# Kernel tuning notes

Measured on AMD Instinct MI355X. Metric: run time of the kernel, lower is better.

## Reference

```python
import math
import jax, jax.numpy as jnp
import numpy as np

NUM_HEADS = 8
EMBED_DIM = 512   # embed_dim_per_head(64) * num_heads(8)
LATENT = 256
HIDDEN = 512
INPUT_DIM = 128
P = 3             # function 'Q' -> 3 polynomial coefficients


def setup_inputs() -> dict:
    key = jax.random.key(0)
    ks = jax.random.split(key, 16)
    B, L, T, D, E = 64, 2048, 1024, INPUT_DIM, EMBED_DIM
    s = lambda fan_in: 1.0 / math.sqrt(fan_in)
    inp = {
        "timesteps": jax.random.uniform(ks[0], (B, L), jnp.float32),
        "X": jax.random.normal(ks[1], (B, L, D), jnp.float32),
        "M": jax.random.bernoulli(ks[2], 0.5, (B, L, D)).astype(jnp.float32),
        "y_time_steps": jax.random.uniform(ks[3], (B, T), jnp.float32),
        # time_embedding: Linear(1, E)
        "w_te": jax.random.normal(ks[4], (E,), jnp.float32),
        "b_te": jnp.zeros((E,), jnp.float32),
        # learned query [1, P, E]
        "query": jax.random.normal(ks[5], (1, P, E), jnp.float32),
        # query_map / key_map: Linear(E, E), stored [in, out]
        "W_q": jax.random.normal(ks[6], (E, E), jnp.float32) * s(E),
        "b_q": jnp.zeros((E,), jnp.float32),
        "W_k": jax.random.normal(ks[7], (E, E), jnp.float32) * s(E),
        "b_k": jnp.zeros((E,), jnp.float32),
        # attn out: Linear(2*D*H, latent)
        "W_o": jax.random.normal(ks[8], (2 * D * NUM_HEADS, LATENT), jnp.float32) * s(2 * D * NUM_HEADS),
        "b_o": jnp.zeros((LATENT,), jnp.float32),
        # decoder MLP: latent -> hidden -> hidden -> D
        "W1": jax.random.normal(ks[9], (LATENT, HIDDEN), jnp.float32) * s(LATENT),
        "b1": jnp.zeros((HIDDEN,), jnp.float32),
        "W2": jax.random.normal(ks[10], (HIDDEN, HIDDEN), jnp.float32) * s(HIDDEN),
        "b2": jnp.zeros((HIDDEN,), jnp.float32),
        "W3": jax.random.normal(ks[11], (HIDDEN, D), jnp.float32) * s(HIDDEN),
        "b3": jnp.zeros((D,), jnp.float32),
    }
    return inp


def _fld_forward(timesteps, X, M, y_time_steps, w_te, b_te, query,
                 W_q, b_q, W_k, b_k, W_o, b_o, W1, b1, W2, b2, W3, b3):
    B, L = timesteps.shape
    D = X.shape[-1]
    E, H = EMBED_DIM, NUM_HEADS
    ek = E // H
    # learn_time_embedding: Linear(1,E) then sin on indices range(0, E, H)
    key = timesteps[..., None] * w_te + b_te                      # [B,L,E]
    sin_mask = (jnp.arange(E) % H) == 0
    key = jnp.where(sin_mask, jnp.sin(key), key)
    Xcat = jnp.concatenate([X, M], axis=-1)                       # [B,L,2D]
    Mcat = jnp.concatenate([M, M], axis=-1)                       # [B,L,2D]
    # mask is used only for masked_fill in torch (no grad through it)
    maskb = jax.lax.stop_gradient((Mcat != 0).astype(Xcat.dtype))
    q = jnp.broadcast_to(query, (B, P, E)) @ W_q + b_q            # [B,P,E]
    k = key @ W_k + b_k                                            # [B,L,E]
    qh = q.reshape(B, P, H, ek).transpose(0, 2, 1, 3)             # [B,H,P,ek]
    kh = k.reshape(B, L, H, ek).transpose(0, 2, 1, 3)             # [B,H,L,ek]
    scores = jnp.einsum('bhpe,bhle->bhpl', qh, kh) / math.sqrt(ek)
    # per-channel masked softmax over L, factorized (masked entries -> exp(-1e9)=0)
    m = jnp.max(scores, axis=-1, keepdims=True)
    w = jnp.exp(scores - m)                                        # [B,H,P,L]
    num = jnp.einsum('bhpl,blc->bhpc', w, maskb * Xcat)            # [B,H,P,2D]
    den = jnp.einsum('bhpl,blc->bhpc', w, maskb)
    x = num / den                                                  # [B,H,P,2D]
    x = x.transpose(0, 2, 1, 3).reshape(B, P, H * 2 * D)
    coeffs = x @ W_o + b_o                                         # [B,P,latent]
    t = y_time_steps[..., None]                                    # [B,T,1]
    c0 = coeffs[:, 0:1, :]
    c1 = coeffs[:, 1:2, :]
    c2 = coeffs[:, 2:3, :]
    z = c0 + t * c1 + (t * t) * c2                                 # [B,T,latent]
    h1 = jax.nn.relu(z @ W1 + b1)
    h2 = jax.nn.relu(h1 @ W2 + b2)
    return h2 @ W3 + b3                                            # [B,T,D]


def reference(timesteps, X, M, y_time_steps, w_te, b_te, query,
              W_q, b_q, W_k, b_k, W_o, b_o, W1, b1, W2, b2, W3, b3):
    return _fld_forward(timesteps, X, M, y_time_steps, w_te, b_te, query,
                        W_q, b_q, W_k, b_k, W_o, b_o, W1, b1, W2, b2, W3, b3)
```

## Files before the change

### kernel.cpp

```cpp
#include <hip/hip_runtime.h>
#include <math.h>

#define NH   8
#define PP   3
#define HP   24
#define E    512
#define EK   64
#define D    128
#define LL   2048
#define BB   64
#define TT   1024
#define LAT  256
#define HID  512
#define CH   8
#define CL   256

typedef __attribute__((ext_vector_type(8))) short bf16x8;
typedef __attribute__((ext_vector_type(4))) float f32x4;
typedef __attribute__((ext_vector_type(16))) float f32x16;

#define OFF_VS     ((size_t)2048)
#define OFF_WA     ((size_t)4096)
#define OFF_WB     ((size_t)4128)
#define OFF_SB     ((size_t)4160)
#define OFF_CVP    ((size_t)73728)
#define OFF_P2     ((size_t)81920)
#define OFF_PART   ((size_t)475136)
#define OFF_SC     ((size_t)3620864)
#define OFF_A      ((size_t)3784704)

__device__ inline ushort f2bf(float x) {
    union { float f; uint u; } v; v.f = x;
    uint r = v.u + 0x7fffu + ((v.u >> 16) & 1u);
    return (ushort)(r >> 16);
}
__device__ inline uint swz(uint a)  { return a ^ (((a >> 8) & 7u) << 4); }
__device__ inline uint swzH(uint a) { return a ^ (((a >> 7) & 7u) << 4); }
__device__ inline uint swzQ(uint a) { return a ^ (((a >> 9) & 7u) << 4); }
__device__ inline uint pk2(float lo, float hi) {
    return (uint)f2bf(lo) | ((uint)f2bf(hi) << 16);
}
__device__ inline float h1f(float a0, float a1, float a2, float t) {
    return fmaxf(fmaf(t, fmaf(t, a2, a1), a0), 0.f);
}
__device__ inline int sigma(int s) { return s ^ (((((s >> 2) ^ (s >> 3)) & 1)) ? 12 : 0); }

__global__ __launch_bounds__(512) void k_setup(const float* __restrict__ query,
                                               const float* __restrict__ W_q,
                                               const float* __restrict__ b_q,
                                               const float* __restrict__ W_k,
                                               const float* __restrict__ b_k,
                                               const float* __restrict__ w_te,
                                               const float* __restrict__ b_te,
                                               const float* __restrict__ W_o,
                                               const float* __restrict__ W2,
                                               const float* __restrict__ W3,
                                               float* __restrict__ vsin,
                                               float* __restrict__ wA,
                                               float* __restrict__ wB,
                                               float* __restrict__ sbias,
                                               float* __restrict__ cvp,
                                               ushort* __restrict__ W2F,
                                               ushort* __restrict__ W3F) {
    int bx = blockIdx.x, tid = threadIdx.x;
    if (bx < HP) {
        int hp = bx, h = hp / PP, p = hp % PP;
        __shared__ float q_s[EK];
        if (tid < EK) {
            float acc = b_q[h * EK + tid];
            for (int i = 0; i < E; ++i)
                acc += query[p * E + i] * W_q[(size_t)i * E + h * EK + tid];
            q_s[tid] = acc;
        }
        __syncthreads();
        int e = tid;
        const float scale = 0.125f;
        float acc = 0.f;
        for (int j = 0; j < EK; ++j)
            acc += W_k[(size_t)e * E + h * EK + j] * q_s[j];
        float v = acc * scale;
        if ((e & 7) == 0) vsin[hp * 64 + (e >> 3)] = v;
        __shared__ float r1[512], r2[512];
        r1[e] = v * w_te[e];
        r2[e] = v * b_te[e];
        __syncthreads();
        for (int s = 256; s > 0; s >>= 1) {
            if (e < s) { r1[e] += r1[e + s]; r2[e] += r2[e + s]; }
            __syncthreads();
        }
        if (e == 0) {
            wA[hp] = r1[0];
            wB[hp] = r2[0];
            float sb = 0.f;
            for (int j = 0; j < EK; ++j) sb += b_k[h * EK + j] * q_s[j];
            sbias[hp] = sb * scale;
        }
    } else if (bx < HP + 32) {
        int bc = bx - HP;
        int h = bc >> 2, cc = bc & 3, o = tid & 255;
        float acc = 0.f;
        #pragma unroll 8
        for (int c = cc * 32; c < cc * 32 + 32; ++c)
            acc += W_o[(size_t)(h * 256 + 128 + c) * LAT + o];
        cvp[(h * 4 + cc) * LAT + o] = acc;
    } else {
        int gid = (bx - HP - 32) * 512 + tid;
        int l = gid & 63;
        int kb = 8 * (l >> 5);
        int cb = l & 31;
        if (gid < 32768) {
            int F = gid >> 6;
            int JT = F & 15, ks = F >> 4;
            int cbp = sigma(cb);
            int k0 = ks * 16 + kb, j = JT * 32 + cbp;
            #pragma unroll
            for (int e = 0; e < 8; ++e)
                W2F[(size_t)gid * 8 + e] = f2bf(W2[(size_t)(k0 + e) * HID + j]);
        } else {
            int g2 = gid - 32768;
            int F2 = g2 >> 6;
            int CT = F2 & 3, KT = F2 >> 2;
            int k0 = KT * 16 + kb, c = CT * 32 + cb;
            #pragma unroll
            for (int e = 0; e < 8; ++e)
                W3F[(size_t)g2 * 8 + e] = f2bf(W3[(size_t)(k0 + e) * D + c]);
        }
    }
}

__global__ __launch_bounds__(512, 6) void k_wsf(const float* __restrict__ timesteps,
                                                const float* __restrict__ w_te,
                                                const float* __restrict__ b_te,
                                                const float* __restrict__ vsin,
                                                const float* __restrict__ wA,
                                                const float* __restrict__ wB,
                                                const float* __restrict__ sb,
                                                const float* __restrict__ X,
                                                const float* __restrict__ M,
                                                float* __restrict__ part) {
    __shared__ char sbuf[49152];
    float* vs_s = (float*)sbuf;
    float* w8_s = (float*)(sbuf + 6144);
    float* b8_s = (float*)(sbuf + 6400);
    float* wA_s = (float*)(sbuf + 6656);
    float* wB_s = (float*)(sbuf + 6784);
    float* sb_s = (float*)(sbuf + 6912);
    ushort* vt  = (ushort*)sbuf;
    ushort* w_s = (ushort*)(sbuf + 32768);
    int b = blockIdx.x / CH, ch = blockIdx.x % CH;
    int l0 = ch * CL;
    int tid = threadIdx.x;

    for (int i = tid; i < HP * 64; i += 512) vs_s[i] = vsin[i];
    if (tid < 64) { w8_s[tid] = w_te[tid * 8]; b8_s[tid] = b_te[tid * 8]; }
    if (tid < HP) { wA_s[tid] = wA[tid]; wB_s[tid] = wB[tid]; sb_s[tid] = sb[tid]; }
    __syncthreads();

    {
        int lpair = tid & 127, hh = tid >> 7;
        float ts0 = timesteps[(size_t)b * LL + l0 + lpair * 2];
        float ts1 = timesteps[(size_t)b * LL + l0 + lpair * 2 + 1];
        float sc0[6], sc1[6];
        #pragma unroll
        for (int i = 0; i < 6; ++i) {
            int hp = hh * 6 + i;
            sc0[i] = fmaf(ts0, wA_s[hp], wB_s[hp]) + sb_s[hp];
            sc1[i] = fmaf(ts1, wA_s[hp], wB_s[hp]) + sb_s[hp];
        }
        for (int jc = 0; jc < 64; jc += 8) {
            float d0[8], d1[8];
            #pragma unroll
            for (int j = 0; j < 8; ++j) {
                float w = w8_s[jc + j], bb = b8_s[jc + j];
                float k0 = fmaf(ts0, w, bb), k1 = fmaf(ts1, w, bb);
                d0[j] = __sinf(k0) - k0;
                d1[j] = __sinf(k1) - k1;
            }
            #pragma unroll
            for (int i = 0; i < 6; ++i) {
                int hp = hh * 6 + i;
                #pragma unroll
                for (int j = 0; j < 8; j += 4) {
                    float4 v4 = *(const float4*)&vs_s[hp * 64 + jc + j];
                    sc0[i] += d0[j] * v4.x + d0[j+1] * v4.y + d0[j+2] * v4.z + d0[j+3] * v4.w;
                    sc1[i] += d1[j] * v4.x + d1[j+1] * v4.y + d1[j+2] * v4.z + d1[j+3] * v4.w;
                }
            }
        }
        #pragma unroll
        for (int i = 0; i < 6; ++i) {
            int hp = hh * 6 + i;
            *(uint*)((char*)w_s + swzQ((uint)(hp * 512 + lpair * 4))) = pk2(__expf(sc0[i]), __expf(sc1[i]));
        }
        for (int idx = tid; idx < 8 * 128; idx += 512) {
            int hp = 24 + (idx >> 7), lp = idx & 127;
            *(uint*)((char*)w_s + swzQ((uint)(hp * 512 + lp * 4))) = 0u;
        }
    }
    __syncthreads();

    int lane = tid & 63, wv = tid >> 6;
    int l31 = lane & 31, hl = lane >> 5;
    f32x16 acc;
    #pragma unroll
    for (int e = 0; e < 16; ++e) acc[e] = 0.f;

    int cst = tid & 127, lg = tid >> 7;
    for (int q = 0; q < 4; ++q) {
        if (q) __syncthreads();
        #pragma unroll
        for (int i = 0; i < 8; ++i) {
            int ll = lg * 16 + i * 2;
            size_t g0 = ((size_t)b * LL + l0 + q * 64 + ll) * D + cst;
            float m0 = M[g0], m1 = M[g0 + D];
            float x0 = X[g0] * m0, x1 = X[g0 + D] * m1;
            *(uint*)((char*)vt + swzH((uint)(cst * 128 + ll * 2)))         = pk2(x0, x1);
            *(uint*)((char*)vt + swzH((uint)((128 + cst) * 128 + ll * 2))) = pk2(m0, m1);
        }
        __syncthreads();
        #pragma unroll
        for (int ks = 0; ks < 4; ++ks) {
            bf16x8 af = *(const bf16x8*)((char*)w_s + swzQ((uint)(l31 * 512 + (q * 64 + ks * 16 + hl * 8) * 2)));
            bf16x8 bf_ = *(const bf16x8*)((char*)vt + swzH((uint)((wv * 32 + l31) * 128 + (ks * 16 + hl * 8) * 2)));
            acc = __builtin_amdgcn_mfma_f32_32x32x16_bf16(af, bf_, acc, 0, 0, 0);
        }
    }
    size_t base = ((size_t)(b * CH + ch) * HP) * 256;
    #pragma unroll
    for (int reg = 0; reg < 12; ++reg) {
        int hp = (reg & 3) + 8 * (reg >> 2) + 4 * hl;
        part[base + (size_t)hp * 256 + wv * 32 + l31] = acc[reg];
    }
}

__global__ __launch_bounds__(256) void k_mid(const float* __restrict__ part,
                                             const float* __restrict__ W_o,
                                             float* __restrict__ part2) {
    int bx = blockIdx.x, tid = threadIdx.x;
    int b = bx >> 3, h = bx & 7;
    __shared__ float ratio[PP][D];
    for (int ii = tid; ii < PP * D; ii += 256) {
        int p = ii >> 7, c = ii & 127;
        int hp = h * PP + p;
        float n = 0.f, d = 0.f;
        for (int ch = 0; ch < CH; ++ch) {
            size_t base = ((size_t)(b * CH + ch) * HP + hp) * 256;
            n += part[base + c];
            d += part[base + 128 + c];
        }
        ratio[p][c] = n / d;
    }
    __syncthreads();
    int o = tid;
    float a0 = 0.f, a1 = 0.f, a2 = 0.f;
    #pragma unroll 4
    for (int c = 0; c < D; ++c) {
        float w = W_o[(size_t)(h * 256 + c) * LAT + o];
        a0 = fmaf(ratio[0][c], w, a0);
        a1 = fmaf(ratio[1][c], w, a1);
        a2 = fmaf(ratio[2][c], w, a2);
    }
    size_t base = (((size_t)b * NH + h) * PP) * LAT + o;
    part2[base]           = a0;
    part2[base + LAT]     = a1;
    part2[base + 2 * LAT] = a2;
}

__global__ __launch_bounds__(128) void k_avec4(const float* __restrict__ part2,
                                               const float* __restrict__ cvp,
                                               const float* __restrict__ b_o,
                                               const float* __restrict__ W1,
                                               const float* __restrict__ b1,
                                               float* __restrict__ abuf) {
    int b = blockIdx.x, jq = blockIdx.y, tid = threadIdx.x;
    __shared__ float cf[PP * LAT];
    for (int idx = tid; idx < PP * LAT; idx += 128) {
        int p = idx / LAT, o = idx % LAT;
        float s = b_o[o];
        #pragma unroll 8
        for (int i = 0; i < 32; ++i) s += cvp[i * LAT + o];
        for (int h = 0; h < NH; ++h)
            s += part2[(((size_t)b * NH + h) * PP + p) * LAT + o];
        cf[p * LAT + o] = s;
    }
    __syncthreads();
    int j = jq * 128 + tid;
    float a0 = b1[j], a1 = 0.f, a2 = 0.f;
    #pragma unroll 4
    for (int k = 0; k < LAT; ++k) {
        float w = W1[(size_t)k * HID + j];
        a0 = fmaf(cf[k], w, a0);
        a1 = fmaf(cf[LAT + k], w, a1);
        a2 = fmaf(cf[2 * LAT + k], w, a2);
    }
    abuf[(size_t)b * 3 * HID + j] = a0;
    abuf[(size_t)b * 3 * HID + HID + j] = a1;
    abuf[(size_t)b * 3 * HID + 2 * HID + j] = a2;
}

__global__ __launch_bounds__(512, 4) void k_mlp12(const float* __restrict__ abuf,
                                                  const float* __restrict__ yts,
                                                  const ushort* __restrict__ W2F,
                                                  const float* __restrict__ b2,
                                                  const ushort* __restrict__ W3F,
                                                  const float* __restrict__ b3,
                                                  float* __restrict__ out) {
    __shared__ char lds[65536];
    int b = blockIdx.x, t0 = blockIdx.y * 64, tid = threadIdx.x;
    const float* a0p = abuf + (size_t)b * 3 * HID;
    const float* a1p = a0p + HID;
    const float* a2p = a1p + HID;

    {
        int sr = tid & 63, sub0 = (tid >> 6) & 1, skp = tid >> 7;
        float t = yts[(size_t)b * TT + t0 + sr];
        int kg0 = skp * 128 + sub0 * 64;
        uint sbase = (uint)(skp * 16384 + sr * 256 + sub0 * 128);
        #pragma unroll
        for (int i = 0; i < 8; ++i) {
            int k = kg0 + i * 8;
            float4 xa0 = *(const float4*)(a0p + k), xb0 = *(const float4*)(a0p + k + 4);
            float4 xa1 = *(const float4*)(a1p + k), xb1 = *(const float4*)(a1p + k + 4);
            float4 xa2 = *(const float4*)(a2p + k), xb2 = *(const float4*)(a2p + k + 4);
            uint4 pk;
            pk.x = pk2(h1f(xa0.x, xa1.x, xa2.x, t), h1f(xa0.y, xa1.y, xa2.y, t));
            pk.y = pk2(h1f(xa0.z, xa1.z, xa2.z, t), h1f(xa0.w, xa1.w, xa2.w, t));
            pk.z = pk2(h1f(xb0.x, xb1.x, xb2.x, t), h1f(xb0.y, xb1.y, xb2.y, t));
            pk.w = pk2(h1f(xb0.z, xb1.z, xb2.z, t), h1f(xb0.w, xb1.w, xb2.w, t));
            *(uint4*)(lds + swz(sbase + i * 16)) = pk;
        }
    }
    __syncthreads();

    int lane = tid & 63, w = tid >> 6;
    int l31 = lane & 31, hl = lane >> 5;
    int wp = w & 1, gw = w >> 1;
    int Jb = gw * 4 + wp * 2;

    f32x16 acc[2][2];
    #pragma unroll
    for (int jt = 0; jt < 2; ++jt) {
        int jT = (Jb + jt) * 32;
        #pragma unroll
        for (int reg = 0; reg < 16; ++reg) {
            int slot = (reg & 3) + 8 * (reg >> 2) + 4 * hl;
            float bv = b2[jT + sigma(slot)];
            acc[jt][0][reg] = bv;
            acc[jt][1][reg] = bv;
        }
    }
    #pragma unroll 4
    for (int ks = 0; ks < 32; ++ks) {
        uint base = (uint)((ks >> 3) * 16384 + (ks & 7) * 32 + hl * 16);
        bf16x8 bh0 = *(const bf16x8*)(lds + swz(base + (uint)(l31 * 256)));
        bf16x8 bh1 = *(const bf16x8*)(lds + swz(base + (uint)((32 + l31) * 256)));
        #pragma unroll
        for (int jt = 0; jt < 2; ++jt) {
            bf16x8 af = *(const bf16x8*)(W2F + ((size_t)(ks * 16 + Jb + jt) * 64 + lane) * 8);
            acc[jt][0] = __builtin_amdgcn_mfma_f32_32x32x16_bf16(af, bh0, acc[jt][0], 0, 0, 0);
            acc[jt][1] = __builtin_amdgcn_mfma_f32_32x32x16_bf16(af, bh1, acc[jt][1], 0, 0, 0);
        }
    }
    __syncthreads();

    #pragma unroll
    for (int jt = 0; jt < 2; ++jt) {
        int J = Jb + jt;
        #pragma unroll
        for (int rtile = 0; rtile < 2; ++rtile)
            #pragma unroll
            for (int s = 0; s < 2; ++s) {
                uint4 uu;
                uu.x = pk2(fmaxf(acc[jt][rtile][8 * s + 0], 0.f), fmaxf(acc[jt][rtile][8 * s + 1], 0.f));
                uu.y = pk2(fmaxf(acc[jt][rtile][8 * s + 2], 0.f), fmaxf(acc[jt][rtile][8 * s + 3], 0.f));
                uu.z = pk2(fmaxf(acc[jt][rtile][8 * s + 4], 0.f), fmaxf(acc[jt][rtile][8 * s + 5], 0.f));
                uu.w = pk2(fmaxf(acc[jt][rtile][8 * s + 6], 0.f), fmaxf(acc[jt][rtile][8 * s + 7], 0.f));
                *(uint4*)(lds + (uint)((rtile * 32 + J * 2 + s) * 1024 + lane * 16)) = uu;
            }
    }
    __syncthreads();

    f32x16 acc2a, acc2b;
    {
        float bv = b3[gw * 32 + l31];
        #pragma unroll
        for (int e = 0; e < 16; ++e) { acc2a[e] = bv; acc2b[e] = 0.f; }
    }
    #pragma unroll 4
    for (int sg = 0; sg < 32; sg += 2) {
        {
            bf16x8 ah = *(const bf16x8*)(lds + (uint)((wp * 32 + sg) * 1024 + lane * 16));
            bf16x8 bw = *(const bf16x8*)(W3F + ((size_t)(sg * 4 + gw) * 64 + lane) * 8);
            acc2a = __builtin_amdgcn_mfma_f32_32x32x16_bf16(ah, bw, acc2a, 0, 0, 0);
        }
        {
            bf16x8 ah = *(const bf16x8*)(lds + (uint)((wp * 32 + sg + 1) * 1024 + lane * 16));
            bf16x8 bw = *(const bf16x8*)(W3F + ((size_t)((sg + 1) * 4 + gw) * 64 + lane) * 8);
            acc2b = __builtin_amdgcn_mfma_f32_32x32x16_bf16(ah, bw, acc2b, 0, 0, 0);
        }
    }

    {
        int c = gw * 32 + l31;
        size_t rowbase = (size_t)b * TT + t0 + wp * 32 + 4 * hl;
        #pragma unroll
        for (int reg = 0; reg < 16; ++reg)
            out[(rowbase + (reg & 3) + 8 * (reg >> 2)) * D + c] = acc2a[reg] + acc2b[reg];
    }
}

extern "C" void kernel_launch(void* const* d_in, const int* in_sizes, int n_in,
                              void* d_out, int out_size, void* d_ws, size_t ws_size,
                              hipStream_t stream) {
    const float* timesteps = (const float*)d_in[0];
    const float* X        = (const float*)d_in[1];
    const float* M        = (const float*)d_in[2];
    const float* yts      = (const float*)d_in[3];
    const float* w_te     = (const float*)d_in[4];
    const float* b_te     = (const float*)d_in[5];
    const float* query    = (const float*)d_in[6];
    const float* W_q      = (const float*)d_in[7];
    const float* b_q      = (const float*)d_in[8];
    const float* W_k      = (const float*)d_in[9];
    const float* b_k      = (const float*)d_in[10];
    const float* W_o      = (const float*)d_in[11];
    const float* b_o      = (const float*)d_in[12];
    const float* W1       = (const float*)d_in[13];
    const float* b1       = (const float*)d_in[14];
    const float* W2       = (const float*)d_in[15];
    const float* b2       = (const float*)d_in[16];
    const float* W3       = (const float*)d_in[17];
    const float* b3       = (const float*)d_in[18];
    float* out = (float*)d_out;
    float* ws  = (float*)d_ws;

    float* vsin   = ws + OFF_VS;
    float* wA     = ws + OFF_WA;
    float* wB     = ws + OFF_WB;
    float* sbias  = ws + OFF_SB;
    float* cvp    = ws + OFF_CVP;
    float* part2  = ws + OFF_P2;
    float* part   = ws + OFF_PART;
    float* abuf   = ws + OFF_A;
    ushort* W2F   = (ushort*)(ws + OFF_SC);
    ushort* W3F   = W2F + (size_t)HID * HID;

    hipLaunchKernelGGL(k_setup,  dim3(HP + 32 + 80),  dim3(512), 0, stream,
                       query, W_q, b_q, W_k, b_k, w_te, b_te, W_o, W2, W3,
                       vsin, wA, wB, sbias, cvp, W2F, W3F);
    hipLaunchKernelGGL(k_wsf,    dim3(BB * CH),       dim3(512), 0, stream,
                       timesteps, w_te, b_te, vsin, wA, wB, sbias, X, M, part);
    hipLaunchKernelGGL(k_mid,    dim3(BB * NH),       dim3(256), 0, stream,
                       part, W_o, part2);
    hipLaunchKernelGGL(k_avec4,  dim3(BB, 4),         dim3(128), 0, stream,
                       part2, cvp, b_o, W1, b1, abuf);
    hipLaunchKernelGGL(k_mlp12,  dim3(BB, TT / 64),   dim3(512), 0, stream,
                       abuf, yts, W2F, b2, W3F, b3, out);
}
```

Before: 159.7 us.

## Split sequence into 16 chunks per batch and store partial sums in bf16

```diff
diff --git a/kernel.cpp b/kernel.cpp
--- a/kernel.cpp
+++ b/kernel.cpp
@@ -12,11 +12,9 @@
 #define TT   1024
 #define LAT  256
 #define HID  512
-#define CH   8
-#define CL   256
+#define CH2  16
 
 typedef __attribute__((ext_vector_type(8))) short bf16x8;
-typedef __attribute__((ext_vector_type(4))) float f32x4;
 typedef __attribute__((ext_vector_type(16))) float f32x16;
 
 #define OFF_VS     ((size_t)2048)
@@ -34,9 +32,12 @@
     uint r = v.u + 0x7fffu + ((v.u >> 16) & 1u);
     return (ushort)(r >> 16);
 }
+__device__ inline float bf2f(ushort u) {
+    union { uint u; float f; } v; v.u = (uint)u << 16;
+    return v.f;
+}
 __device__ inline uint swz(uint a)  { return a ^ (((a >> 8) & 7u) << 4); }
 __device__ inline uint swzH(uint a) { return a ^ (((a >> 7) & 7u) << 4); }
-__device__ inline uint swzQ(uint a) { return a ^ (((a >> 9) & 7u) << 4); }
 __device__ inline uint pk2(float lo, float hi) {
     return (uint)f2bf(lo) | ((uint)f2bf(hi) << 16);
 }
@@ -128,17 +129,17 @@
     }
 }
 
-__global__ __launch_bounds__(512, 6) void k_wsf(const float* __restrict__ timesteps,
-                                                const float* __restrict__ w_te,
-                                                const float* __restrict__ b_te,
-                                                const float* __restrict__ vsin,
-                                                const float* __restrict__ wA,
-                                                const float* __restrict__ wB,
-                                                const float* __restrict__ sb,
-                                                const float* __restrict__ X,
-                                                const float* __restrict__ M,
-                                                float* __restrict__ part) {
-    __shared__ char sbuf[49152];
+__global__ __launch_bounds__(512, 8) void k_wsf2(const float* __restrict__ timesteps,
+                                                 const float* __restrict__ w_te,
+                                                 const float* __restrict__ b_te,
+                                                 const float* __restrict__ vsin,
+                                                 const float* __restrict__ wA,
+                                                 const float* __restrict__ wB,
+                                                 const float* __restrict__ sb,
+                                                 const float* __restrict__ X,
+                                                 const float* __restrict__ M,
+                                                 ushort* __restrict__ part) {
+    __shared__ char sbuf[40960];
     float* vs_s = (float*)sbuf;
     float* w8_s = (float*)(sbuf + 6144);
     float* b8_s = (float*)(sbuf + 6400);
@@ -147,8 +148,8 @@
     float* sb_s = (float*)(sbuf + 6912);
     ushort* vt  = (ushort*)sbuf;
     ushort* w_s = (ushort*)(sbuf + 32768);
-    int b = blockIdx.x / CH, ch = blockIdx.x % CH;
-    int l0 = ch * CL;
+    int b = blockIdx.x >> 4, ch = blockIdx.x & 15;
+    int l0 = ch * 128;
     int tid = threadIdx.x;
 
     for (int i = tid; i < HP * 64; i += 512) vs_s[i] = vsin[i];
@@ -157,13 +158,13 @@
     __syncthreads();
 
     {
-        int lpair = tid & 127, hh = tid >> 7;
+        int lpair = tid & 63, hh = tid >> 6;
         float ts0 = timesteps[(size_t)b * LL + l0 + lpair * 2];
         float ts1 = timesteps[(size_t)b * LL + l0 + lpair * 2 + 1];
-        float sc0[6], sc1[6];
-        #pragma unroll
-        for (int i = 0; i < 6; ++i) {
-            int hp = hh * 6 + i;
+        float sc0[3], sc1[3];
+        #pragma unroll
+        for (int i = 0; i < 3; ++i) {
+            int hp = hh * 3 + i;
             sc0[i] = fmaf(ts0, wA_s[hp], wB_s[hp]) + sb_s[hp];
             sc1[i] = fmaf(ts1, wA_s[hp], wB_s[hp]) + sb_s[hp];
         }
@@ -177,8 +178,8 @@
                 d1[j] = __sinf(k1) - k1;
             }
             #pragma unroll
-            for (int i = 0; i < 6; ++i) {
-                int hp = hh * 6 + i;
+            for (int i = 0; i < 3; ++i) {
+                int hp = hh * 3 + i;
                 #pragma unroll
                 for (int j = 0; j < 8; j += 4) {
                     float4 v4 = *(const float4*)&vs_s[hp * 64 + jc + j];
@@ -188,14 +189,12 @@
             }
         }
         #pragma unroll
-        for (int i = 0; i < 6; ++i) {
-            int hp = hh * 6 + i;
-            *(uint*)((char*)w_s + swzQ((uint)(hp * 512 + lpair * 4))) = pk2(__expf(sc0[i]), __expf(sc1[i]));
-        }
-        for (int idx = tid; idx < 8 * 128; idx += 512) {
-            int hp = 24 + (idx >> 7), lp = idx & 127;
-            *(uint*)((char*)w_s + swzQ((uint)(hp * 512 + lp * 4))) = 0u;
-        }
+        for (int i = 0; i < 3; ++i) {
+            int hp = hh * 3 + i;
+            *(uint*)((char*)w_s + swz((uint)(hp * 256 + lpair * 4))) = pk2(__expf(sc0[i]), __expf(sc1[i]));
+        }
+        int hp = 24 + (tid >> 6), lp = tid & 63;
+        *(uint*)((char*)w_s + swz((uint)(hp * 256 + lp * 4))) = 0u;
     }
     __syncthreads();
 
@@ -206,7 +205,7 @@
     for (int e = 0; e < 16; ++e) acc[e] = 0.f;
 
     int cst = tid & 127, lg = tid >> 7;
-    for (int q = 0; q < 4; ++q) {
+    for (int q = 0; q < 2; ++q) {
         if (q) __syncthreads();
         #pragma unroll
         for (int i = 0; i < 8; ++i) {
@@ -220,20 +219,20 @@
         __syncthreads();
         #pragma unroll
         for (int ks = 0; ks < 4; ++ks) {
-            bf16x8 af = *(const bf16x8*)((char*)w_s + swzQ((uint)(l31 * 512 + (q * 64 + ks * 16 + hl * 8) * 2)));
+            bf16x8 af = *(const bf16x8*)((char*)w_s + swz((uint)(l31 * 256 + (q * 64 + ks * 16 + hl * 8) * 2)));
             bf16x8 bf_ = *(const bf16x8*)((char*)vt + swzH((uint)((wv * 32 + l31) * 128 + (ks * 16 + hl * 8) * 2)));
             acc = __builtin_amdgcn_mfma_f32_32x32x16_bf16(af, bf_, acc, 0, 0, 0);
         }
     }
-    size_t base = ((size_t)(b * CH + ch) * HP) * 256;
+    size_t base = ((size_t)(b * CH2 + ch) * HP) * 256;
     #pragma unroll
     for (int reg = 0; reg < 12; ++reg) {
         int hp = (reg & 3) + 8 * (reg >> 2) + 4 * hl;
-        part[base + (size_t)hp * 256 + wv * 32 + l31] = acc[reg];
-    }
-}
-
-__global__ __launch_bounds__(256) void k_mid(const float* __restrict__ part,
+        part[base + (size_t)hp * 256 + wv * 32 + l31] = f2bf(acc[reg]);
+    }
+}
+
+__global__ __launch_bounds__(256) void k_mid(const ushort* __restrict__ part,
                                              const float* __restrict__ W_o,
                                              float* __restrict__ part2) {
     int bx = blockIdx.x, tid = threadIdx.x;
@@ -243,10 +242,10 @@
         int p = ii >> 7, c = ii & 127;
         int hp = h * PP + p;
         float n = 0.f, d = 0.f;
-        for (int ch = 0; ch < CH; ++ch) {
-            size_t base = ((size_t)(b * CH + ch) * HP + hp) * 256;
-            n += part[base + c];
-            d += part[base + 128 + c];
+        for (int ch = 0; ch < CH2; ++ch) {
+            size_t base = ((size_t)(b * CH2 + ch) * HP + hp) * 256;
+            n += bf2f(part[base + c]);
+            d += bf2f(part[base + 128 + c]);
         }
         ratio[p][c] = n / d;
     }
@@ -440,7 +439,7 @@
     float* sbias  = ws + OFF_SB;
     float* cvp    = ws + OFF_CVP;
     float* part2  = ws + OFF_P2;
-    float* part   = ws + OFF_PART;
+    ushort* part  = (ushort*)(ws + OFF_PART);
     float* abuf   = ws + OFF_A;
     ushort* W2F   = (ushort*)(ws + OFF_SC);
     ushort* W3F   = W2F + (size_t)HID * HID;
@@ -448,7 +447,7 @@
     hipLaunchKernelGGL(k_setup,  dim3(HP + 32 + 80),  dim3(512), 0, stream,
                        query, W_q, b_q, W_k, b_k, w_te, b_te, W_o, W2, W3,
                        vsin, wA, wB, sbias, cvp, W2F, W3F);
-    hipLaunchKernelGGL(k_wsf,    dim3(BB * CH),       dim3(512), 0, stream,
+    hipLaunchKernelGGL(k_wsf2,   dim3(BB * CH2),      dim3(512), 0, stream,
                        timesteps, w_te, b_te, vsin, wA, wB, sbias, X, M, part);
     hipLaunchKernelGGL(k_mid,    dim3(BB * NH),       dim3(256), 0, stream,
                        part, W_o, part2);
```

New measurement: 154.9 us. -3.0%, faster.
